# Kernel optimization log

Hardware: AMD Instinct MI355X
Metric: run time of the kernel (lower is better)

## Reference

```python
import jax, jax.numpy as jnp
import numpy as np

N_NODES = 100000
N_EDGES = 1600000
N_UNARY = 16
N_BINARY = 4
# Each clause: (literal column indices, signs); sign=-1 means negated literal.
# KENN t-conorm boost: delta = w * sign * softmax(sign * preactivation over clause literals)
UNARY_CLAUSES = [([0, 1], [-1.0, 1.0]),
                 ([2, 3], [-1.0, 1.0]),
                 ([4, 5, 6], [-1.0, 1.0, 1.0]),
                 ([7, 8], [1.0, -1.0])]
# Joined matrix columns: [0:16]=1.P*, [16:32]=2.P*, [32:36]=R*
BINARY_CLAUSES = [([0, 32, 16], [-1.0, -1.0, 1.0]),   # n1.P0, nR0, 2.P0
                  ([1, 33, 17], [-1.0, -1.0, 1.0]),   # n1.P1, nR1, 2.P1
                  ([34, 35], [-1.0, 1.0]),            # nR2, R3
                  ([2, 18], [-1.0, 1.0])]             # n1.P2, 2.P2


def _knowledge_enhancer(x, clauses, weights):
    """Sum of per-clause deltas scattered back into full predicate space."""
    delta = jnp.zeros_like(x)
    for ci, (idx, signs) in enumerate(clauses):
        idx = np.asarray(idx)
        s = jnp.asarray(signs, dtype=x.dtype)
        sel = x[:, idx] * s                                  # [n, L] signed literal preactivations
        d = s * jax.nn.softmax(sel, axis=1) * weights[ci]    # [n, L]
        delta = delta.at[:, idx].add(d)
    return delta


def setup_inputs() -> dict:
    key = jax.random.key(0)
    k1, k2, k3, k4 = jax.random.split(key, 4)
    return {
        "unary": jax.random.normal(k1, (N_NODES, N_UNARY), jnp.float32),
        "binary": jax.random.normal(k2, (N_EDGES, N_BINARY), jnp.float32),
        "index1": jax.random.randint(k3, (N_EDGES,), 0, N_NODES),
        "index2": jax.random.randint(k4, (N_EDGES,), 0, N_NODES),
        "unary_cw": jnp.full((len(UNARY_CLAUSES),), 0.5, jnp.float32),
        "binary_cw": jnp.full((len(BINARY_CLAUSES),), 0.5, jnp.float32),
    }


def reference(unary, binary, index1, index2, unary_cw, binary_cw):
    # unary KnowledgeEnhancer
    u = unary + _knowledge_enhancer(unary, UNARY_CLAUSES, unary_cw)
    # Join: gather unary features for both endpoints of each edge
    joined = jnp.concatenate([u[index1], u[index2], binary], axis=1)  # [m, 2U+B]
    # binary KnowledgeEnhancer over joined matrix
    db = _knowledge_enhancer(joined, BINARY_CLAUSES, binary_cw)
    # GroupBy: scatter-reduce unary parts back to nodes
    delta_up = (jax.ops.segment_sum(db[:, :N_UNARY], index1, num_segments=N_NODES)
                + jax.ops.segment_sum(db[:, N_UNARY:2 * N_UNARY], index2, num_segments=N_NODES))
    delta_bp = db[:, 2 * N_UNARY:]
    # activation is identity (default)
    return u + delta_up, binary + delta_bp
```

## Files before the change

### kernel.cpp

```cpp
#include <hip/hip_runtime.h>
#include <math.h>

#define N_NODES 100000
#define N_EDGES 1600000
#define N_UNARY 16

#define NCHUNK 8
#define CH 12500
#define NWG_E 6250
#define CAP 128
#define CAP_SHIFT 7
#define NSLICE 32
#define PER_SLICE 196

#define FPSCALE 8192.0f
#define INV_FPSCALE (1.0f / 8192.0f)

typedef unsigned long long u64;

__device__ inline long long pack3(float a, float b, float c) {
    long long qa = (long long)__float2int_rn(a * FPSCALE);
    long long qb = (long long)__float2int_rn(b * FPSCALE);
    long long qc = (long long)__float2int_rn(c * FPSCALE);
    return (qa << 42) + (qb << 21) + qc;
}

__device__ inline u64 enc_rec(int local, float a, float b, float c) {
    int qa = __float2int_rn(a * FPSCALE);
    int qb = __float2int_rn(b * FPSCALE);
    int qc = __float2int_rn(c * FPSCALE);
    return ((u64)local << 42) |
           ((u64)((unsigned)qa & 0x3FFFu) << 28) |
           ((u64)((unsigned)qb & 0x3FFFu) << 14) |
           ((u64)((unsigned)qc & 0x3FFFu));
}

__global__ __launch_bounds__(256) void kenn_node_kernel(
    const float* __restrict__ unary,
    const float* __restrict__ ucw,
    float* __restrict__ out_nodes,
    float4* __restrict__ u3tab,
    u64* __restrict__ acc,
    int ncopies)
{
    int n = blockIdx.x * blockDim.x + threadIdx.x;
    if (n >= N_NODES) return;

    for (int x = 0; x < ncopies; ++x)
        acc[(size_t)x * N_NODES + n] = 0ull;

    const float w0 = ucw[0], w1 = ucw[1], w2 = ucw[2], w3 = ucw[3];

    const float4* row = reinterpret_cast<const float4*>(unary + (size_t)n * N_UNARY);
    float4 r0 = row[0], r1 = row[1], r2 = row[2], r3 = row[3];

    float x0 = r0.x, x1 = r0.y, x2 = r0.z, x3 = r0.w;
    float x4 = r1.x, x5 = r1.y, x6 = r1.z, x7 = r1.w;
    float x8 = r2.x;

    {
        float t = __expf(-x0 - x1);
        float p1 = 1.0f / (1.0f + t);
        float p0 = 1.0f - p1;
        x0 = r0.x - w0 * p0;
        x1 = r0.y + w0 * p1;
    }
    {
        float t = __expf(-x2 - x3);
        float p1 = 1.0f / (1.0f + t);
        float p0 = 1.0f - p1;
        x2 = r0.z - w1 * p0;
        x3 = r0.w + w1 * p1;
    }
    {
        float s0 = -x4, s1 = x5, s2 = x6;
        float m = fmaxf(fmaxf(s0, s1), s2);
        float e0 = __expf(s0 - m), e1 = __expf(s1 - m), e2 = __expf(s2 - m);
        float inv = 1.0f / (e0 + e1 + e2);
        x4 = r1.x - w2 * e0 * inv;
        x5 = r1.y + w2 * e1 * inv;
        x6 = r1.z + w2 * e2 * inv;
    }
    {
        float t = __expf(-x8 - x7);
        float p0 = 1.0f / (1.0f + t);
        float p1 = 1.0f - p0;
        x7 = r1.w + w3 * p0;
        x8 = r2.x - w3 * p1;
    }

    float4* orow = reinterpret_cast<float4*>(out_nodes + (size_t)n * N_UNARY);
    orow[0] = make_float4(x0, x1, x2, x3);
    orow[1] = make_float4(x4, x5, x6, x7);
    orow[2] = make_float4(x8, r2.y, r2.z, r2.w);
    orow[3] = r3;

    u3tab[n] = make_float4(x0, x1, x2, x3);
}

__device__ inline void edge_math(float4 a, float4 b, float4 bin,
                                 float w0, float w1, float w2, float w3,
                                 float4& bout,
                                 float& d1c0, float& d1c1, float& d1c2,
                                 float& d2c0, float& d2c1, float& d2c2)
{
    float dbin0, dbin1, dbin2, dbin3;
    {
        float s0 = -a.x, s1 = -bin.x, s2 = b.x;
        float m = fmaxf(fmaxf(s0, s1), s2);
        float e0 = __expf(s0 - m), e1 = __expf(s1 - m), e2 = __expf(s2 - m);
        float inv = 1.0f / (e0 + e1 + e2);
        d1c0  = -w0 * e0 * inv;
        dbin0 = -w0 * e1 * inv;
        d2c0  =  w0 * e2 * inv;
    }
    {
        float s0 = -a.y, s1 = -bin.y, s2 = b.y;
        float m = fmaxf(fmaxf(s0, s1), s2);
        float e0 = __expf(s0 - m), e1 = __expf(s1 - m), e2 = __expf(s2 - m);
        float inv = 1.0f / (e0 + e1 + e2);
        d1c1  = -w1 * e0 * inv;
        dbin1 = -w1 * e1 * inv;
        d2c1  =  w1 * e2 * inv;
    }
    {
        float t = __expf(-bin.z - bin.w);
        float p1 = 1.0f / (1.0f + t);
        float p0 = 1.0f - p1;
        dbin2 = -w2 * p0;
        dbin3 =  w2 * p1;
    }
    {
        float t = __expf(-a.z - b.z);
        float p1 = 1.0f / (1.0f + t);
        float p0 = 1.0f - p1;
        d1c2 = -w3 * p0;
        d2c2 =  w3 * p1;
    }
    bout = make_float4(bin.x + dbin0, bin.y + dbin1, bin.z + dbin2, bin.w + dbin3);
}

__global__ __launch_bounds__(256) void kenn_edge_bin_kernel(
    const float* __restrict__ binary,
    const int* __restrict__ idx1,
    const int* __restrict__ idx2,
    const float* __restrict__ bcw,
    const float4* __restrict__ u3tab,
    u64* __restrict__ rec,
    unsigned int* __restrict__ counts,
    float* __restrict__ out_binary)
{
    __shared__ unsigned int cnt[NCHUNK];
    __shared__ u64 stg[NCHUNK * CAP];

    if (threadIdx.x < NCHUNK) cnt[threadIdx.x] = 0;
    __syncthreads();

    const int e = blockIdx.x * 256 + threadIdx.x;
    const float w0 = bcw[0], w1 = bcw[1], w2 = bcw[2], w3 = bcw[3];

    int i1 = idx1[e];
    int i2 = idx2[e];
    float4 bin = reinterpret_cast<const float4*>(binary)[e];
    float4 a = u3tab[i1];
    float4 b = u3tab[i2];

    float4 bout;
    float d1c0, d1c1, d1c2, d2c0, d2c1, d2c2;
    edge_math(a, b, bin, w0, w1, w2, w3, bout, d1c0, d1c1, d1c2, d2c0, d2c1, d2c2);

    reinterpret_cast<float4*>(out_binary)[e] = bout;

    {
        int c = i1 / CH;
        u64 r = enc_rec(i1 - c * CH, d1c0, d1c1, d1c2);
        unsigned slot = atomicAdd(&cnt[c], 1u);
        if (slot < CAP) stg[(c << CAP_SHIFT) + slot] = r;
    }
    {
        int c = i2 / CH;
        u64 r = enc_rec(i2 - c * CH, d2c0, d2c1, d2c2);
        unsigned slot = atomicAdd(&cnt[c], 1u);
        if (slot < CAP) stg[(c << CAP_SHIFT) + slot] = r;
    }
    __syncthreads();

    const size_t wg = blockIdx.x;
    for (int c = 0; c < NCHUNK; ++c) {
        unsigned n = min(cnt[c], (unsigned)CAP);
        for (unsigned i = threadIdx.x; i < n; i += 256)
            rec[((wg * NCHUNK + c) << CAP_SHIFT) + i] = stg[(c << CAP_SHIFT) + i];
    }
    if (threadIdx.x < NCHUNK)
        counts[wg * NCHUNK + threadIdx.x] = min(cnt[threadIdx.x], (unsigned)CAP);
}

__global__ __launch_bounds__(1024) void kenn_accum_kernel(
    const u64* __restrict__ rec,
    const unsigned int* __restrict__ counts,
    u64* __restrict__ partial)
{
    extern __shared__ u64 accL[];
    __shared__ unsigned int cnts[PER_SLICE];

    const int wg = blockIdx.x;
    const int c = wg >> 5;
    const int s = wg & (NSLICE - 1);
    const int pbase = s * PER_SLICE;
    const int pend = min(pbase + PER_SLICE, NWG_E);
    const int np = pend - pbase;

    for (int j = threadIdx.x; j < np; j += blockDim.x)
        cnts[j] = counts[(size_t)(pbase + j) * NCHUNK + c];
    for (int i = threadIdx.x; i < CH; i += blockDim.x)
        accL[i] = 0ull;
    __syncthreads();

    const int wave = threadIdx.x >> 6;
    const int lane = threadIdx.x & 63;
    for (int j = wave; j < np; j += 16) {
        const int cnt = (int)cnts[j];
        const u64* rp = rec + (((size_t)(pbase + j) * NCHUNK + c) << CAP_SHIFT);
        for (int i = lane; i < cnt; i += 64) {
            u64 r = rp[i];
            int local = (int)(r >> 42);
            long long q0 = (long long)(((long long)(r << 22)) >> 50);
            long long q1 = (long long)(((long long)(r << 36)) >> 50);
            long long q2 = (long long)(((long long)(r << 50)) >> 50);
            u64 pkt = (u64)((q0 << 42) + (q1 << 21) + q2);
            atomicAdd(&accL[local], pkt);
        }
    }
    __syncthreads();

    u64* pout = partial + (size_t)wg * CH;
    for (int i = threadIdx.x; i < CH; i += blockDim.x)
        pout[i] = accL[i];
}

__global__ __launch_bounds__(256) void kenn_final_kernel(
    const u64* __restrict__ partial,
    const float4* __restrict__ u3tab,
    float* __restrict__ out_nodes)
{
    int n = blockIdx.x * blockDim.x + threadIdx.x;
    if (n >= N_NODES) return;

    int c = n / CH;
    int local = n - c * CH;
    const u64* pp = partial + (size_t)(c * NSLICE) * CH + local;

    long long t = 0;
#pragma unroll
    for (int s = 0; s < NSLICE; ++s)
        t += (long long)pp[(size_t)s * CH];

    long long qc = (t << 43) >> 43;
    t = (t - qc) >> 21;
    long long qb = (t << 43) >> 43;
    long long qa = (t - qb) >> 21;

    float4 u = u3tab[n];
    reinterpret_cast<float4*>(out_nodes + (size_t)n * N_UNARY)[0] =
        make_float4(u.x + (float)qa * INV_FPSCALE,
                    u.y + (float)qb * INV_FPSCALE,
                    u.z + (float)qc * INV_FPSCALE,
                    u.w);
}

__global__ __launch_bounds__(256) void kenn_edge_atomic_kernel(
    const float* __restrict__ binary,
    const int* __restrict__ idx1,
    const int* __restrict__ idx2,
    const float* __restrict__ bcw,
    const float4* __restrict__ u3tab,
    u64* __restrict__ acc,
    float* __restrict__ out_binary)
{
    int e = blockIdx.x * blockDim.x + threadIdx.x;
    if (e >= N_EDGES) return;

    const float w0 = bcw[0], w1 = bcw[1], w2 = bcw[2], w3 = bcw[3];

    int i1 = idx1[e];
    int i2 = idx2[e];
    float4 bin = reinterpret_cast<const float4*>(binary)[e];
    float4 a = u3tab[i1];
    float4 b = u3tab[i2];

    float4 bout;
    float d1c0, d1c1, d1c2, d2c0, d2c1, d2c2;
    edge_math(a, b, bin, w0, w1, w2, w3, bout, d1c0, d1c1, d1c2, d2c0, d2c1, d2c2);

    reinterpret_cast<float4*>(out_binary)[e] = bout;

    atomicAdd(&acc[i1], (u64)pack3(d1c0, d1c1, d1c2));
    atomicAdd(&acc[i2], (u64)pack3(d2c0, d2c1, d2c2));
}

__global__ __launch_bounds__(256) void kenn_fixup_kernel(
    const u64* __restrict__ acc,
    const float4* __restrict__ u3tab,
    float* __restrict__ out_nodes)
{
    int n = blockIdx.x * blockDim.x + threadIdx.x;
    if (n >= N_NODES) return;

    long long t = (long long)acc[n];
    long long qc = (t << 43) >> 43;
    t = (t - qc) >> 21;
    long long qb = (t << 43) >> 43;
    long long qa = (t - qb) >> 21;

    float4 u = u3tab[n];
    reinterpret_cast<float4*>(out_nodes + (size_t)n * N_UNARY)[0] =
        make_float4(u.x + (float)qa * INV_FPSCALE,
                    u.y + (float)qb * INV_FPSCALE,
                    u.z + (float)qc * INV_FPSCALE,
                    u.w);
}

extern "C" void kernel_launch(void* const* d_in, const int* in_sizes, int n_in,
                              void* d_out, int out_size, void* d_ws, size_t ws_size,
                              hipStream_t stream) {
    const float* unary    = (const float*)d_in[0];
    const float* binary   = (const float*)d_in[1];
    const int*   index1   = (const int*)d_in[2];
    const int*   index2   = (const int*)d_in[3];
    const float* unary_cw = (const float*)d_in[4];
    const float* bin_cw   = (const float*)d_in[5];

    float* out_nodes  = (float*)d_out;
    float* out_binary = (float*)d_out + (size_t)N_NODES * N_UNARY;

    char* base = (char*)d_ws;
    size_t off_u3   = 0;
    size_t off_rec  = off_u3 + (size_t)N_NODES * 16;
    size_t off_cnt  = off_rec + (size_t)NWG_E * NCHUNK * CAP * 8;
    size_t off_par  = (off_cnt + (size_t)NWG_E * NCHUNK * 4 + 255) & ~(size_t)255;
    size_t need     = off_par + (size_t)NCHUNK * NSLICE * CH * 8;

    float4* u3tab = (float4*)(base + off_u3);

    dim3 blockN(256), gridN((N_NODES + 255) / 256);
    dim3 blockE(256), gridE(NWG_E);

    if (ws_size >= need) {
        u64* rec = (u64*)(base + off_rec);
        unsigned int* counts = (unsigned int*)(base + off_cnt);
        u64* partials = (u64*)(base + off_par);

        kenn_node_kernel<<<gridN, blockN, 0, stream>>>(
            unary, unary_cw, out_nodes, u3tab, (u64*)nullptr, 0);

        kenn_edge_bin_kernel<<<gridE, blockE, 0, stream>>>(
            binary, index1, index2, bin_cw, u3tab, rec, counts, out_binary);

        kenn_accum_kernel<<<dim3(NCHUNK * NSLICE), dim3(1024), CH * 8, stream>>>(
            rec, counts, partials);

        kenn_final_kernel<<<gridN, blockN, 0, stream>>>(partials, u3tab, out_nodes);
    } else {
        u64* acc = (u64*)(base + (size_t)N_NODES * 16);
        kenn_node_kernel<<<gridN, blockN, 0, stream>>>(
            unary, unary_cw, out_nodes, u3tab, acc, 1);
        kenn_edge_atomic_kernel<<<gridE, blockE, 0, stream>>>(
            binary, index1, index2, bin_cw, u3tab, acc, out_binary);
        kenn_fixup_kernel<<<gridN, blockN, 0, stream>>>(acc, u3tab, out_nodes);
    }
}
```

Measured before the change: 54.84 us.

## Process two edges per thread, use finer node chunks, add overflow spill

Each thread in the edge kernel now handles two edges, and node chunks go from 8 to 16 with fewer slices. Local-memory accumulators and staging buckets shrink as a result, and the extra independent work per thread aims to raise occupancy and hide latency. Staging records that overflow a bucket's capacity are now added to a per-node global accumulator with atomics instead of being silently dropped, and the final kernel folds that spill buffer in. The node kernel now always zeroes the spill buffer, and the overflow path adds global atomic traffic when buckets fill.

Result: faster. 52.75 us (-3.8%).

```diff
diff --git a/kernel.cpp b/kernel.cpp
--- a/kernel.cpp
+++ b/kernel.cpp
@@ -5,12 +5,12 @@
 #define N_EDGES 1600000
 #define N_UNARY 16
 
-#define NCHUNK 8
-#define CH 12500
-#define NWG_E 6250
-#define CAP 128
-#define CAP_SHIFT 7
-#define NSLICE 32
+#define NCHUNK 16
+#define CH 6250
+#define EPW 512
+#define NWG_E 3125
+#define CAP 112
+#define NSLICE 16
 #define PER_SLICE 196
 
 #define FPSCALE 8192.0f
@@ -35,19 +35,31 @@
            ((u64)((unsigned)qc & 0x3FFFu));
 }
 
+__device__ inline void stage_rec(int node, float d0, float d1, float d2,
+                                 unsigned int* __restrict__ cnt,
+                                 u64* __restrict__ stg,
+                                 u64* __restrict__ spill)
+{
+    int c = node / CH;
+    int local = node - c * CH;
+    unsigned slot = atomicAdd(&cnt[c], 1u);
+    if (slot < CAP)
+        stg[c * CAP + slot] = enc_rec(local, d0, d1, d2);
+    else
+        atomicAdd(&spill[node], (u64)pack3(d0, d1, d2));
+}
+
 __global__ __launch_bounds__(256) void kenn_node_kernel(
     const float* __restrict__ unary,
     const float* __restrict__ ucw,
     float* __restrict__ out_nodes,
     float4* __restrict__ u3tab,
-    u64* __restrict__ acc,
-    int ncopies)
+    u64* __restrict__ acc)
 {
     int n = blockIdx.x * blockDim.x + threadIdx.x;
     if (n >= N_NODES) return;
 
-    for (int x = 0; x < ncopies; ++x)
-        acc[(size_t)x * N_NODES + n] = 0ull;
+    acc[n] = 0ull;
 
     const float w0 = ucw[0], w1 = ucw[1], w2 = ucw[2], w3 = ucw[3];
 
@@ -148,6 +160,7 @@
     const float4* __restrict__ u3tab,
     u64* __restrict__ rec,
     unsigned int* __restrict__ counts,
+    u64* __restrict__ spill,
     float* __restrict__ out_binary)
 {
     __shared__ unsigned int cnt[NCHUNK];
@@ -156,40 +169,44 @@
     if (threadIdx.x < NCHUNK) cnt[threadIdx.x] = 0;
     __syncthreads();
 
-    const int e = blockIdx.x * 256 + threadIdx.x;
     const float w0 = bcw[0], w1 = bcw[1], w2 = bcw[2], w3 = bcw[3];
 
-    int i1 = idx1[e];
-    int i2 = idx2[e];
-    float4 bin = reinterpret_cast<const float4*>(binary)[e];
-    float4 a = u3tab[i1];
-    float4 b = u3tab[i2];
-
-    float4 bout;
-    float d1c0, d1c1, d1c2, d2c0, d2c1, d2c2;
-    edge_math(a, b, bin, w0, w1, w2, w3, bout, d1c0, d1c1, d1c2, d2c0, d2c1, d2c2);
-
-    reinterpret_cast<float4*>(out_binary)[e] = bout;
-
-    {
-        int c = i1 / CH;
-        u64 r = enc_rec(i1 - c * CH, d1c0, d1c1, d1c2);
-        unsigned slot = atomicAdd(&cnt[c], 1u);
-        if (slot < CAP) stg[(c << CAP_SHIFT) + slot] = r;
-    }
-    {
-        int c = i2 / CH;
-        u64 r = enc_rec(i2 - c * CH, d2c0, d2c1, d2c2);
-        unsigned slot = atomicAdd(&cnt[c], 1u);
-        if (slot < CAP) stg[(c << CAP_SHIFT) + slot] = r;
-    }
+    const int e0 = blockIdx.x * EPW + threadIdx.x;
+    const int e1 = e0 + 256;
+
+    int i1a = idx1[e0], i2a = idx2[e0];
+    int i1b = idx1[e1], i2b = idx2[e1];
+    float4 bina = reinterpret_cast<const float4*>(binary)[e0];
+    float4 binb = reinterpret_cast<const float4*>(binary)[e1];
+    float4 aa = u3tab[i1a];
+    float4 ba = u3tab[i2a];
+    float4 ab = u3tab[i1b];
+    float4 bb = u3tab[i2b];
+
+    float4 bouta, boutb;
+    float a1c0, a1c1, a1c2, a2c0, a2c1, a2c2;
+    float b1c0, b1c1, b1c2, b2c0, b2c1, b2c2;
+    edge_math(aa, ba, bina, w0, w1, w2, w3, bouta, a1c0, a1c1, a1c2, a2c0, a2c1, a2c2);
+    edge_math(ab, bb, binb, w0, w1, w2, w3, boutb, b1c0, b1c1, b1c2, b2c0, b2c1, b2c2);
+
+    reinterpret_cast<float4*>(out_binary)[e0] = bouta;
+    reinterpret_cast<float4*>(out_binary)[e1] = boutb;
+
+    stage_rec(i1a, a1c0, a1c1, a1c2, cnt, stg, spill);
+    stage_rec(i2a, a2c0, a2c1, a2c2, cnt, stg, spill);
+    stage_rec(i1b, b1c0, b1c1, b1c2, cnt, stg, spill);
+    stage_rec(i2b, b2c0, b2c1, b2c2, cnt, stg, spill);
     __syncthreads();
 
     const size_t wg = blockIdx.x;
-    for (int c = 0; c < NCHUNK; ++c) {
+    const int wv = threadIdx.x >> 6;
+    const int ln = threadIdx.x & 63;
+#pragma unroll
+    for (int j = 0; j < 4; ++j) {
+        int c = wv * 4 + j;
         unsigned n = min(cnt[c], (unsigned)CAP);
-        for (unsigned i = threadIdx.x; i < n; i += 256)
-            rec[((wg * NCHUNK + c) << CAP_SHIFT) + i] = stg[(c << CAP_SHIFT) + i];
+        for (unsigned i = ln; i < n; i += 64)
+            rec[((wg * NCHUNK + c) * CAP) + i] = stg[c * CAP + i];
     }
     if (threadIdx.x < NCHUNK)
         counts[wg * NCHUNK + threadIdx.x] = min(cnt[threadIdx.x], (unsigned)CAP);
@@ -204,7 +221,7 @@
     __shared__ unsigned int cnts[PER_SLICE];
 
     const int wg = blockIdx.x;
-    const int c = wg >> 5;
+    const int c = wg >> 4;
     const int s = wg & (NSLICE - 1);
     const int pbase = s * PER_SLICE;
     const int pend = min(pbase + PER_SLICE, NWG_E);
@@ -220,13 +237,13 @@
     const int lane = threadIdx.x & 63;
     for (int j = wave; j < np; j += 16) {
         const int cnt = (int)cnts[j];
-        const u64* rp = rec + (((size_t)(pbase + j) * NCHUNK + c) << CAP_SHIFT);
+        const u64* rp = rec + ((size_t)(pbase + j) * NCHUNK + c) * CAP;
         for (int i = lane; i < cnt; i += 64) {
             u64 r = rp[i];
             int local = (int)(r >> 42);
-            long long q0 = (long long)(((long long)(r << 22)) >> 50);
-            long long q1 = (long long)(((long long)(r << 36)) >> 50);
-            long long q2 = (long long)(((long long)(r << 50)) >> 50);
+            long long q0 = ((long long)(r << 22)) >> 50;
+            long long q1 = ((long long)(r << 36)) >> 50;
+            long long q2 = ((long long)(r << 50)) >> 50;
             u64 pkt = (u64)((q0 << 42) + (q1 << 21) + q2);
             atomicAdd(&accL[local], pkt);
         }
@@ -240,6 +257,7 @@
 
 __global__ __launch_bounds__(256) void kenn_final_kernel(
     const u64* __restrict__ partial,
+    const u64* __restrict__ spill,
     const float4* __restrict__ u3tab,
     float* __restrict__ out_nodes)
 {
@@ -250,7 +268,7 @@
     int local = n - c * CH;
     const u64* pp = partial + (size_t)(c * NSLICE) * CH + local;
 
-    long long t = 0;
+    long long t = (long long)spill[n];
 #pragma unroll
     for (int s = 0; s < NSLICE; ++s)
         t += (long long)pp[(size_t)s * CH];
@@ -335,36 +353,35 @@
 
     char* base = (char*)d_ws;
     size_t off_u3   = 0;
-    size_t off_rec  = off_u3 + (size_t)N_NODES * 16;
+    size_t off_acc  = off_u3 + (size_t)N_NODES * 16;
+    size_t off_rec  = off_acc + (size_t)N_NODES * 8;
     size_t off_cnt  = off_rec + (size_t)NWG_E * NCHUNK * CAP * 8;
     size_t off_par  = (off_cnt + (size_t)NWG_E * NCHUNK * 4 + 255) & ~(size_t)255;
     size_t need     = off_par + (size_t)NCHUNK * NSLICE * CH * 8;
 
     float4* u3tab = (float4*)(base + off_u3);
+    u64* acc = (u64*)(base + off_acc);
 
     dim3 blockN(256), gridN((N_NODES + 255) / 256);
-    dim3 blockE(256), gridE(NWG_E);
+
+    kenn_node_kernel<<<gridN, blockN, 0, stream>>>(unary, unary_cw, out_nodes,
+                                                   u3tab, acc);
 
     if (ws_size >= need) {
         u64* rec = (u64*)(base + off_rec);
         unsigned int* counts = (unsigned int*)(base + off_cnt);
         u64* partials = (u64*)(base + off_par);
 
-        kenn_node_kernel<<<gridN, blockN, 0, stream>>>(
-            unary, unary_cw, out_nodes, u3tab, (u64*)nullptr, 0);
-
-        kenn_edge_bin_kernel<<<gridE, blockE, 0, stream>>>(
-            binary, index1, index2, bin_cw, u3tab, rec, counts, out_binary);
+        kenn_edge_bin_kernel<<<dim3(NWG_E), dim3(256), 0, stream>>>(
+            binary, index1, index2, bin_cw, u3tab, rec, counts, acc, out_binary);
 
         kenn_accum_kernel<<<dim3(NCHUNK * NSLICE), dim3(1024), CH * 8, stream>>>(
             rec, counts, partials);
 
-        kenn_final_kernel<<<gridN, blockN, 0, stream>>>(partials, u3tab, out_nodes);
+        kenn_final_kernel<<<gridN, blockN, 0, stream>>>(partials, acc, u3tab,
+                                                        out_nodes);
     } else {
-        u64* acc = (u64*)(base + (size_t)N_NODES * 16);
-        kenn_node_kernel<<<gridN, blockN, 0, stream>>>(
-            unary, unary_cw, out_nodes, u3tab, acc, 1);
-        kenn_edge_atomic_kernel<<<gridE, blockE, 0, stream>>>(
+        kenn_edge_atomic_kernel<<<dim3((N_EDGES + 255) / 256), dim3(256), 0, stream>>>(
             binary, index1, index2, bin_cw, u3tab, acc, out_binary);
         kenn_fixup_kernel<<<gridN, blockN, 0, stream>>>(acc, u3tab, out_nodes);
     }
```
